# Kernel tuning notes

Measured on AMD Instinct MI355X. Metric: run time of the kernel, lower is better.

Reference implementation:

```python
import jax, jax.numpy as jnp
import numpy as np

EPS = 1e-6

def _layernorm(x, gamma, beta):
    # normalize over last dim (head_dim)
    mean = x.mean(axis=-1, keepdims=True)
    var = x.var(axis=-1, keepdims=True)
    return gamma * (x - mean) * jax.lax.rsqrt(var + EPS) + beta

def setup_inputs() -> dict:
    key = jax.random.key(0)
    ks = jax.random.split(key, 6)
    B, N, C, H = 2, 2048, 1024, 16
    Dh = C // H
    x = jax.random.normal(ks[0], (B, N, C), dtype=jnp.float32)
    qkv_w = jax.random.normal(ks[1], (C, 3 * C), dtype=jnp.float32) * (1.0 / np.sqrt(C))
    q_gamma = jnp.ones((Dh,), jnp.float32)
    q_beta = jnp.zeros((Dh,), jnp.float32)
    k_gamma = jnp.ones((Dh,), jnp.float32)
    k_beta = jnp.zeros((Dh,), jnp.float32)
    proj_w = jax.random.normal(ks[2], (C, C), dtype=jnp.float32) * (1.0 / np.sqrt(C))
    proj_b = jnp.zeros((C,), jnp.float32)
    return {"x": x, "qkv_w": qkv_w, "q_gamma": q_gamma, "q_beta": q_beta,
            "k_gamma": k_gamma, "k_beta": k_beta, "proj_w": proj_w, "proj_b": proj_b}

def reference(x, qkv_w, q_gamma, q_beta, k_gamma, k_beta, proj_w, proj_b):
    B, N, C = x.shape
    H = 16
    Dh = C // H
    scale = Dh ** -0.5
    qkv = x @ qkv_w                                   # [B,N,3C]
    qkv = qkv.reshape(B, N, 3, H, Dh)
    q = qkv[:, :, 0].transpose(0, 2, 1, 3)            # [B,H,N,Dh]
    k = qkv[:, :, 1].transpose(0, 2, 1, 3)
    v = qkv[:, :, 2].transpose(0, 2, 1, 3)
    q = _layernorm(q, q_gamma, q_beta)
    k = _layernorm(k, k_gamma, k_beta)
    attn = jnp.einsum('bhnd,bhmd->bhnm', q, k) * scale
    attn = jax.nn.softmax(attn, axis=-1)
    out = jnp.einsum('bhnm,bhmd->bhnd', attn, v)      # [B,H,N,Dh]
    out = out.transpose(0, 2, 1, 3).reshape(B, N, C)
    return out @ proj_w + proj_b
```

## Files before the change

### kernel.cpp

```cpp
#include <hip/hip_runtime.h>

typedef unsigned short u16;
typedef unsigned int u32;
typedef float f32x4 __attribute__((ext_vector_type(4)));
typedef float f32x16 __attribute__((ext_vector_type(16)));
typedef short s16x8 __attribute__((ext_vector_type(8)));

#define B_ 2
#define N_ 2048
#define C_ 1024
#define H_ 16
#define BN_ (B_*N_)

#define EXP2F(x) __builtin_amdgcn_exp2f(x)

__device__ __forceinline__ u16 f2bf(float f) {
  union { float f; unsigned u; } c; c.f = f;
  unsigned u = c.u;
  u = (u + 0x7fffu + ((u >> 16) & 1u)) >> 16;
  return (u16)u;
}
__device__ __forceinline__ float bf2f(u16 h) {
  union { unsigned u; float f; } c; c.u = ((unsigned)h) << 16;
  return c.f;
}
__device__ __forceinline__ u32 pack2(float lo, float hi) {
  u32 r;
  asm("v_cvt_pk_bf16_f32 %0, %1, %2" : "=v"(r) : "v"(lo), "v"(hi));
  return r;
}
__device__ __forceinline__ void gload16(const u16* g, u16* l) {
  __builtin_amdgcn_global_load_lds(
      (const __attribute__((address_space(1))) unsigned*)g,
      (__attribute__((address_space(3))) unsigned*)l, 16, 0, 0);
}

__global__ __launch_bounds__(256) void k_cast_bf16(const float* __restrict__ x,
                                                   u16* __restrict__ o, int n4) {
  int i = blockIdx.x * blockDim.x + threadIdx.x;
  if (i >= n4) return;
  float4 v = ((const float4*)x)[i];
  ushort4 r;
  r.x = f2bf(v.x); r.y = f2bf(v.y); r.z = f2bf(v.z); r.w = f2bf(v.w);
  ((ushort4*)o)[i] = r;
}

__global__ __launch_bounds__(256) void k_transpose_cast(const float* __restrict__ W,
                                                        u16* __restrict__ Wt,
                                                        int R, int Cc) {
  __shared__ float t[32][33];
  int tx = threadIdx.x, ty = threadIdx.y;
  int c0 = blockIdx.x * 32, r0 = blockIdx.y * 32;
#pragma unroll
  for (int i = 0; i < 4; ++i)
    t[ty + i * 8][tx] = W[(long)(r0 + ty + i * 8) * Cc + c0 + tx];
  __syncthreads();
#pragma unroll
  for (int i = 0; i < 4; ++i)
    Wt[(long)(c0 + ty + i * 8) * R + r0 + tx] = f2bf(t[tx][ty + i * 8]);
}

__global__ __launch_bounds__(256) void k_gemm_qkv_ln(const u16* __restrict__ A,
                                                     const u16* __restrict__ Bt,
                                                     const float* __restrict__ qg,
                                                     const float* __restrict__ qbeta,
                                                     const float* __restrict__ kg,
                                                     const float* __restrict__ kbeta,
                                                     u16* __restrict__ Qh,
                                                     u16* __restrict__ Kh,
                                                     u16* __restrict__ Vh) {
  const int K = C_;
  __shared__ u16 a_t[2][128 * 64];
  __shared__ u16 b_t[2][128 * 64];
  int tid = threadIdx.x;
  int w = tid >> 6, l = tid & 63;
  int l15 = l & 15, lhi = l >> 4;
  int wm = w >> 1, wn = w & 1;
  int rowA = l >> 3;
  int colA = ((l & 7) ^ (rowA & 7)) * 8;
  int x0 = (lhi ^ (l15 & 7)) * 8;
  int x1 = ((4 + lhi) ^ (l15 & 7)) * 8;
  const u16* Ab = A + (long)blockIdx.y * 128 * K;
  const u16* Bb = Bt + (long)blockIdx.x * 128 * K;
  f32x4 acc[4][4];
#pragma unroll
  for (int m = 0; m < 4; ++m)
#pragma unroll
    for (int n = 0; n < 4; ++n)
      acc[m][n] = (f32x4){0.f, 0.f, 0.f, 0.f};

  auto STAGE = [&](int k0, int bi) {
#pragma unroll
    for (int i = 0; i < 4; ++i) {
      int ci = i * 4 + w;
      gload16(Ab + (long)(ci * 8 + rowA) * K + k0 + colA, &a_t[bi][ci * 512]);
      gload16(Bb + (long)(ci * 8 + rowA) * K + k0 + colA, &b_t[bi][ci * 512]);
    }
  };

  const int NS = K / 64;
  STAGE(0, 0);
  for (int t = 0; t < NS; ++t) {
    __builtin_amdgcn_s_barrier();
    if (t + 1 < NS) {
      STAGE((t + 1) * 64, (t + 1) & 1);
      asm volatile("s_waitcnt vmcnt(8)" ::: "memory");
    } else {
      asm volatile("s_waitcnt vmcnt(0)" ::: "memory");
    }
    __builtin_amdgcn_s_barrier();
    const u16* at = a_t[t & 1];
    const u16* bt = b_t[t & 1];
#pragma unroll
    for (int kk = 0; kk < 2; ++kk) {
      int xo = kk ? x1 : x0;
      s16x8 af[4], bfr[4];
#pragma unroll
      for (int m = 0; m < 4; ++m)
        af[m] = *(const s16x8*)&at[(wm * 64 + m * 16 + l15) * 64 + xo];
#pragma unroll
      for (int n = 0; n < 4; ++n)
        bfr[n] = *(const s16x8*)&bt[(wn * 64 + n * 16 + l15) * 64 + xo];
#pragma unroll
      for (int m = 0; m < 4; ++m)
#pragma unroll
        for (int n = 0; n < 4; ++n)
          acc[m][n] = __builtin_amdgcn_mfma_f32_16x16x32_bf16(af[m], bfr[n], acc[m][n], 0, 0, 0);
    }
  }

  int cb = blockIdx.x * 128 + wn * 64;
  int s = cb >> 10;
  int h = (cb & 1023) >> 6;
  int rowbase = blockIdx.y * 128 + wm * 64;

  if (s == 2) {
#pragma unroll
    for (int m = 0; m < 4; ++m) {
#pragma unroll
      for (int r = 0; r < 4; ++r) {
        int row = rowbase + m * 16 + lhi * 4 + r;
        int b = row >> 11, nn = row & (N_ - 1);
        long ob = ((long)(b * H_ + h) * N_ + nn) * 64;
#pragma unroll
        for (int n = 0; n < 4; ++n)
          Vh[ob + n * 16 + l15] = f2bf(acc[m][n][r]);
      }
    }
  } else {
    const float* g = (s == 0) ? qg : kg;
    const float* be = (s == 0) ? qbeta : kbeta;
    u16* Oh = (s == 0) ? Qh : Kh;
    float sc = (s == 0) ? 0.125f * 1.44269504089f : 1.f;
    float gv[4], bv[4];
#pragma unroll
    for (int n = 0; n < 4; ++n) { gv[n] = g[n * 16 + l15]; bv[n] = be[n * 16 + l15]; }
#pragma unroll
    for (int m = 0; m < 4; ++m) {
#pragma unroll
      for (int r = 0; r < 4; ++r) {
        float t = (acc[m][0][r] + acc[m][1][r]) + (acc[m][2][r] + acc[m][3][r]);
        t += __shfl_xor(t, 1); t += __shfl_xor(t, 2);
        t += __shfl_xor(t, 4); t += __shfl_xor(t, 8);
        float mean = t * (1.f / 64.f);
        float v0 = acc[m][0][r] - mean, v1 = acc[m][1][r] - mean;
        float v2 = acc[m][2][r] - mean, v3 = acc[m][3][r] - mean;
        float q2 = (v0 * v0 + v1 * v1) + (v2 * v2 + v3 * v3);
        q2 += __shfl_xor(q2, 1); q2 += __shfl_xor(q2, 2);
        q2 += __shfl_xor(q2, 4); q2 += __shfl_xor(q2, 8);
        float rs = rsqrtf(q2 * (1.f / 64.f) + 1e-6f);
        int row = rowbase + m * 16 + lhi * 4 + r;
        int b = row >> 11, nn = row & (N_ - 1);
        long ob = ((long)(b * H_ + h) * N_ + nn) * 64;
        float vv[4] = {v0, v1, v2, v3};
#pragma unroll
        for (int n = 0; n < 4; ++n)
          Oh[ob + n * 16 + l15] = f2bf(sc * (gv[n] * vv[n] * rs + bv[n]));
      }
    }
  }
}

__global__ __launch_bounds__(256) void k_gemm_proj(const u16* __restrict__ A,
                                                   const u16* __restrict__ Bt,
                                                   float* __restrict__ Cout,
                                                   const float* __restrict__ bias,
                                                   int M, int N, int K) {
  __shared__ u16 a_t[2][128 * 64];
  __shared__ u16 b_t[2][128 * 64];
  int tid = threadIdx.x;
  int w = tid >> 6, l = tid & 63;
  int l15 = l & 15, lhi = l >> 4;
  int wm = w >> 1, wn = w & 1;
  int rowA = l >> 3;
  int colA = ((l & 7) ^ (rowA & 7)) * 8;
  int x0 = (lhi ^ (l15 & 7)) * 8;
  int x1 = ((4 + lhi) ^ (l15 & 7)) * 8;
  const u16* Ab = A + (long)blockIdx.y * 128 * K;
  const u16* Bb = Bt + (long)blockIdx.x * 128 * K;
  f32x4 acc[4][4];
#pragma unroll
  for (int m = 0; m < 4; ++m)
#pragma unroll
    for (int n = 0; n < 4; ++n)
      acc[m][n] = (f32x4){0.f, 0.f, 0.f, 0.f};

  auto STAGE = [&](int k0, int bi) {
#pragma unroll
    for (int i = 0; i < 4; ++i) {
      int ci = i * 4 + w;
      gload16(Ab + (long)(ci * 8 + rowA) * K + k0 + colA, &a_t[bi][ci * 512]);
      gload16(Bb + (long)(ci * 8 + rowA) * K + k0 + colA, &b_t[bi][ci * 512]);
    }
  };

  const int NS = 1024 / 64;
  STAGE(0, 0);
  for (int t = 0; t < NS; ++t) {
    __builtin_amdgcn_s_barrier();
    if (t + 1 < NS) {
      STAGE((t + 1) * 64, (t + 1) & 1);
      asm volatile("s_waitcnt vmcnt(8)" ::: "memory");
    } else {
      asm volatile("s_waitcnt vmcnt(0)" ::: "memory");
    }
    __builtin_amdgcn_s_barrier();
    const u16* at = a_t[t & 1];
    const u16* bt = b_t[t & 1];
#pragma unroll
    for (int kk = 0; kk < 2; ++kk) {
      int xo = kk ? x1 : x0;
      s16x8 af[4], bfr[4];
#pragma unroll
      for (int m = 0; m < 4; ++m)
        af[m] = *(const s16x8*)&at[(wm * 64 + m * 16 + l15) * 64 + xo];
#pragma unroll
      for (int n = 0; n < 4; ++n)
        bfr[n] = *(const s16x8*)&bt[(wn * 64 + n * 16 + l15) * 64 + xo];
#pragma unroll
      for (int m = 0; m < 4; ++m)
#pragma unroll
        for (int n = 0; n < 4; ++n)
          acc[m][n] = __builtin_amdgcn_mfma_f32_16x16x32_bf16(af[m], bfr[n], acc[m][n], 0, 0, 0);
    }
  }
#pragma unroll
  for (int m = 0; m < 4; ++m) {
#pragma unroll
    for (int n = 0; n < 4; ++n) {
      int col = blockIdx.x * 128 + wn * 64 + n * 16 + l15;
#pragma unroll
      for (int r = 0; r < 4; ++r) {
        int row = blockIdx.y * 128 + wm * 64 + m * 16 + lhi * 4 + r;
        Cout[(long)row * N + col] = acc[m][n][r] + bias[col];
      }
    }
  }
}

__global__ __launch_bounds__(512) void k_transpose_v(const u16* __restrict__ Vh,
                                                     u16* __restrict__ Vt) {
  __shared__ u16 t[64][65];
  int tx = threadIdx.x, ty = threadIdx.y;
  int bh = blockIdx.y;
  int n0 = blockIdx.x * 64;
#pragma unroll
  for (int i = 0; i < 8; ++i)
    t[ty + i * 8][tx] = Vh[((long)bh * N_ + n0 + ty + i * 8) * 64 + tx];
  __syncthreads();
#pragma unroll
  for (int i = 0; i < 8; ++i)
    Vt[((long)bh * 64 + ty + i * 8) * N_ + n0 + tx] = t[tx][ty + i * 8];
}

__global__ __launch_bounds__(512, 4) void k_attn(const u16* __restrict__ Qh,
                                                 const u16* __restrict__ Kh,
                                                 const u16* __restrict__ Vt,
                                                 u16* __restrict__ O) {
  __shared__ u16 k_t[2][2][64 * 64];
  __shared__ u16 v_t[2][2][64 * 64];
  int tid = threadIdx.x;
  int w = tid >> 6, l = tid & 63;
  int half = w >> 2, wq = w & 3;
  int l31 = l & 31, hi = l >> 5;
  int id = blockIdx.x;
  int swz = (id & 7) * 64 + (id >> 3);
  int bh = swz >> 4, qb = swz & 15;
  int b = bh >> 4, h = bh & 15;
  const u16* Qb = Qh + ((long)bh * N_ + qb * 128 + wq * 32) * 64;
  const u16* Kb = Kh + ((long)bh * N_ + half * 1024) * 64;
  const u16* Vb = Vt + (long)bh * 64 * N_ + half * 1024;

  s16x8 qf[4];
#pragma unroll
  for (int j = 0; j < 4; ++j)
    qf[j] = *(const s16x8*)&Qb[l31 * 64 + j * 16 + hi * 8];

  f32x16 acc0, acc1;
#pragma unroll
  for (int i = 0; i < 16; ++i) { acc0[i] = 0.f; acc1[i] = 0.f; }
  float lsum = 0.f;

  int off[2][4];
#pragma unroll
  for (int t = 0; t < 2; ++t)
#pragma unroll
    for (int j = 0; j < 4; ++j)
      off[t][j] = (t * 32 + l31) * 64 + (((j * 2 + hi) ^ (l & 7)) * 8);

  int srow = l >> 3;
  int scol = ((l & 7) ^ srow) * 8;

  auto STAGE = [&](int kt, int bi) {
#pragma unroll
    for (int i = 0; i < 2; ++i) {
      int ci = i * 4 + wq;
      gload16(Kb + (long)(kt + ci * 8 + srow) * 64 + scol, &k_t[half][bi][ci * 512]);
      gload16(Vb + (long)(ci * 8 + srow) * N_ + kt + scol, &v_t[half][bi][ci * 512]);
    }
  };

  const int NT = 16;
  STAGE(0, 0);

  for (int t = 0; t < NT; ++t) {
    __builtin_amdgcn_s_barrier();
    if (t + 1 < NT) {
      STAGE((t + 1) * 64, (t + 1) & 1);
      asm volatile("s_waitcnt vmcnt(4)" ::: "memory");
    } else {
      asm volatile("s_waitcnt vmcnt(0)" ::: "memory");
    }
    __builtin_amdgcn_s_barrier();
    const u16* kb = k_t[half][t & 1];
    const u16* vb = v_t[half][t & 1];

    f32x16 s0, s1;
#pragma unroll
    for (int i = 0; i < 16; ++i) { s0[i] = 0.f; s1[i] = 0.f; }
    __builtin_amdgcn_s_setprio(1);
#pragma unroll
    for (int j = 0; j < 4; ++j) {
      s16x8 kf0 = *(const s16x8*)&kb[off[0][j]];
      s0 = __builtin_amdgcn_mfma_f32_32x32x16_bf16(kf0, qf[j], s0, 0, 0, 0);
      s16x8 kf1 = *(const s16x8*)&kb[off[1][j]];
      s1 = __builtin_amdgcn_mfma_f32_32x32x16_bf16(kf1, qf[j], s1, 0, 0, 0);
    }
    __builtin_amdgcn_s_setprio(0);

#pragma unroll
    for (int i = 0; i < 16; ++i) {
      s0[i] = EXP2F(s0[i]);
      s1[i] = EXP2F(s1[i]);
    }
    f32x16 sm;
#pragma unroll
    for (int i = 0; i < 16; ++i) sm[i] = s0[i] + s1[i];
#pragma unroll
    for (int i = 0; i < 8; ++i) sm[i] += sm[i + 8];
#pragma unroll
    for (int i = 0; i < 4; ++i) sm[i] += sm[i + 4];
    float rs = (sm[0] + sm[1]) + (sm[2] + sm[3]);
    lsum += rs + __shfl_xor(rs, 32);

    s16x8 pa[4];
#pragma unroll
    for (int g = 0; g < 4; ++g) {
      const f32x16& sv = (g < 2) ? s0 : s1;
      int o = (g & 1) * 8;
      u32 w01 = pack2(sv[o + 0], sv[o + 1]);
      u32 w23 = pack2(sv[o + 2], sv[o + 3]);
      u32 w45 = pack2(sv[o + 4], sv[o + 5]);
      u32 w67 = pack2(sv[o + 6], sv[o + 7]);
      u32 recvA = __shfl_xor(hi ? w01 : w45, 32);
      u32 recvB = __shfl_xor(hi ? w23 : w67, 32);
      union { u32 u[4]; s16x8 v; } fr;
      fr.u[0] = hi ? recvA : w01;
      fr.u[1] = hi ? recvB : w23;
      fr.u[2] = hi ? w45 : recvA;
      fr.u[3] = hi ? w67 : recvB;
      pa[g] = fr.v;
    }

    __builtin_amdgcn_s_setprio(1);
#pragma unroll
    for (int j = 0; j < 4; ++j) {
      s16x8 vf0 = *(const s16x8*)&vb[off[0][j]];
      acc0 = __builtin_amdgcn_mfma_f32_32x32x16_bf16(pa[j], vf0, acc0, 0, 0, 0);
      s16x8 vf1 = *(const s16x8*)&vb[off[1][j]];
      acc1 = __builtin_amdgcn_mfma_f32_32x32x16_bf16(pa[j], vf1, acc1, 0, 0, 0);
    }
    __builtin_amdgcn_s_setprio(0);
  }

  __syncthreads();
  float* mbuf = (float*)&k_t[0][0][0];
  float* ml   = (float*)&v_t[0][0][0];

  if (half == 1) {
    if (hi == 0) ml[wq * 32 + l31] = lsum;
#pragma unroll
    for (int r = 0; r < 16; ++r) {
      mbuf[((wq * 32 + r) * 64) + l] = acc0[r];
      mbuf[((wq * 32 + 16 + r) * 64) + l] = acc1[r];
    }
  }
  __syncthreads();

  if (half == 0) {
    float s_b = ml[wq * 32 + l31];
    float lstar = lsum + s_b;
    int lsi = __float_as_int(lstar);
#pragma unroll
    for (int r = 0; r < 16; ++r) {
      int ql = (r & 3) + 8 * (r >> 2) + 4 * hi;
      float ls = __int_as_float(__builtin_amdgcn_ds_bpermute(ql << 2, lsi));
      float o0 = acc0[r] + mbuf[((wq * 32 + r) * 64) + l];
      float o1 = acc1[r] + mbuf[((wq * 32 + 16 + r) * 64) + l];
      float inv = 1.f / ls;
      int q = qb * 128 + wq * 32 + ql;
      long ob = ((long)(b * N_ + q) * H_ + h) * 64 + l31;
      O[ob] = f2bf(o0 * inv);
      O[ob + 32] = f2bf(o1 * inv);
    }
  }
}

extern "C" void kernel_launch(void* const* d_in, const int* in_sizes, int n_in,
                              void* d_out, int out_size, void* d_ws, size_t ws_size,
                              hipStream_t stream) {
  const float* x      = (const float*)d_in[0];
  const float* qkv_w  = (const float*)d_in[1];
  const float* q_g    = (const float*)d_in[2];
  const float* q_b    = (const float*)d_in[3];
  const float* k_g    = (const float*)d_in[4];
  const float* k_b    = (const float*)d_in[5];
  const float* proj_w = (const float*)d_in[6];
  const float* proj_b = (const float*)d_in[7];
  float* out = (float*)d_out;

  char* ws = (char*)d_ws;
  u16* xb     = (u16*)(ws + 0);
  u16* wqkvT  = (u16*)(ws + 8388608);
  u16* wprojT = (u16*)(ws + 14680064);
  u16* Qh     = (u16*)(ws + 16777216);
  u16* Kh     = (u16*)(ws + 25165824);
  u16* Vh     = (u16*)(ws + 33554432);
  u16* Vt     = (u16*)(ws + 41943040);
  u16* attnO  = xb;

  k_cast_bf16<<<4096, 256, 0, stream>>>(x, xb, (BN_ * C_) / 4);
  k_transpose_cast<<<dim3(96, 32), dim3(32, 8), 0, stream>>>(qkv_w, wqkvT, C_, 3 * C_);
  k_transpose_cast<<<dim3(32, 32), dim3(32, 8), 0, stream>>>(proj_w, wprojT, C_, C_);
  k_gemm_qkv_ln<<<dim3(24, 32), 256, 0, stream>>>(xb, wqkvT, q_g, q_b, k_g, k_b, Qh, Kh, Vh);
  k_transpose_v<<<dim3(32, 32), dim3(64, 8), 0, stream>>>(Vh, Vt);
  k_attn<<<512, 512, 0, stream>>>(Qh, Kh, Vt, attnO);
  k_gemm_proj<<<dim3(8, 32), 256, 0, stream>>>(attnO, wprojT, out, proj_b, BN_, C_, C_);
}
```

Baseline: 133.8 us.

## Fuse V transpose into QKV GEMM epilogue via shared-memory staging

The QKV GEMM epilogue for the V slice now stages the accumulator tile in shared memory, reusing the GEMM's LDS buffer, and writes V directly in transposed [bh, d, n] layout with 16-byte stores. This removes the separate transpose kernel launch and the round trip of V through global memory. The cost is an extra block barrier and some LDS traffic in the epilogue of the V blocks. pack2 is assumed to exist in the hidden helper code.

New measurement: 129.6 us. 1.03x faster.

```diff
diff --git a/kernel.cpp b/kernel.cpp
--- a/kernel.cpp
+++ b/kernel.cpp
@@ -68,10 +68,9 @@
                                                      const float* __restrict__ kbeta,
                                                      u16* __restrict__ Qh,
                                                      u16* __restrict__ Kh,
-                                                     u16* __restrict__ Vh) {
+                                                     u16* __restrict__ Vt) {
   const int K = C_;
-  __shared__ u16 a_t[2][128 * 64];
-  __shared__ u16 b_t[2][128 * 64];
+  __shared__ u16 smem[32768];
   int tid = threadIdx.x;
   int w = tid >> 6, l = tid & 63;
   int l15 = l & 15, lhi = l >> 4;
@@ -90,11 +89,13 @@
       acc[m][n] = (f32x4){0.f, 0.f, 0.f, 0.f};
 
   auto STAGE = [&](int k0, int bi) {
+    u16* at = smem + bi * 8192;
+    u16* bt = smem + 16384 + bi * 8192;
 #pragma unroll
     for (int i = 0; i < 4; ++i) {
       int ci = i * 4 + w;
-      gload16(Ab + (long)(ci * 8 + rowA) * K + k0 + colA, &a_t[bi][ci * 512]);
-      gload16(Bb + (long)(ci * 8 + rowA) * K + k0 + colA, &b_t[bi][ci * 512]);
+      gload16(Ab + (long)(ci * 8 + rowA) * K + k0 + colA, &at[ci * 512]);
+      gload16(Bb + (long)(ci * 8 + rowA) * K + k0 + colA, &bt[ci * 512]);
     }
   };
 
@@ -109,8 +110,8 @@
       asm volatile("s_waitcnt vmcnt(0)" ::: "memory");
     }
     __builtin_amdgcn_s_barrier();
-    const u16* at = a_t[t & 1];
-    const u16* bt = b_t[t & 1];
+    const u16* at = smem + (t & 1) * 8192;
+    const u16* bt = smem + 16384 + (t & 1) * 8192;
 #pragma unroll
     for (int kk = 0; kk < 2; ++kk) {
       int xo = kk ? x1 : x0;
@@ -135,17 +136,28 @@
   int rowbase = blockIdx.y * 128 + wm * 64;
 
   if (s == 2) {
-#pragma unroll
-    for (int m = 0; m < 4; ++m) {
-#pragma unroll
-      for (int r = 0; r < 4; ++r) {
-        int row = rowbase + m * 16 + lhi * 4 + r;
-        int b = row >> 11, nn = row & (N_ - 1);
-        long ob = ((long)(b * H_ + h) * N_ + nn) * 64;
-#pragma unroll
-        for (int n = 0; n < 4; ++n)
-          Vh[ob + n * 16 + l15] = f2bf(acc[m][n][r]);
+    __syncthreads();
+    u16* tbuf = smem + w * 4608;
+    u32* tb32 = (u32*)tbuf;
+#pragma unroll
+    for (int m = 0; m < 4; ++m)
+#pragma unroll
+      for (int n = 0; n < 4; ++n) {
+        int d = n * 16 + l15;
+#pragma unroll
+        for (int r = 0; r < 4; r += 2)
+          tb32[d * 36 + m * 8 + lhi * 2 + (r >> 1)] =
+              pack2(acc[m][n][r], acc[m][n][r + 1]);
       }
+    int b = rowbase >> 11;
+    int nnb = rowbase & (N_ - 1);
+    int bhv = b * H_ + h;
+    int ch = (l & 7) * 8;
+#pragma unroll
+    for (int i = 0; i < 8; ++i) {
+      int dl = i * 8 + (l >> 3);
+      s16x8 vv = *(const s16x8*)&tbuf[dl * 72 + ch];
+      *(s16x8*)&Vt[(long)(bhv * 64 + dl) * N_ + nnb + ch] = vv;
     }
   } else {
     const float* g = (s == 0) ? qg : kg;
@@ -258,21 +270,6 @@
   }
 }
 
-__global__ __launch_bounds__(512) void k_transpose_v(const u16* __restrict__ Vh,
-                                                     u16* __restrict__ Vt) {
-  __shared__ u16 t[64][65];
-  int tx = threadIdx.x, ty = threadIdx.y;
-  int bh = blockIdx.y;
-  int n0 = blockIdx.x * 64;
-#pragma unroll
-  for (int i = 0; i < 8; ++i)
-    t[ty + i * 8][tx] = Vh[((long)bh * N_ + n0 + ty + i * 8) * 64 + tx];
-  __syncthreads();
-#pragma unroll
-  for (int i = 0; i < 8; ++i)
-    Vt[((long)bh * 64 + ty + i * 8) * N_ + n0 + tx] = t[tx][ty + i * 8];
-}
-
 __global__ __launch_bounds__(512, 4) void k_attn(const u16* __restrict__ Qh,
                                                  const u16* __restrict__ Kh,
                                                  const u16* __restrict__ Vt,
@@ -445,15 +442,13 @@
   u16* wprojT = (u16*)(ws + 14680064);
   u16* Qh     = (u16*)(ws + 16777216);
   u16* Kh     = (u16*)(ws + 25165824);
-  u16* Vh     = (u16*)(ws + 33554432);
   u16* Vt     = (u16*)(ws + 41943040);
   u16* attnO  = xb;
 
   k_cast_bf16<<<4096, 256, 0, stream>>>(x, xb, (BN_ * C_) / 4);
   k_transpose_cast<<<dim3(96, 32), dim3(32, 8), 0, stream>>>(qkv_w, wqkvT, C_, 3 * C_);
   k_transpose_cast<<<dim3(32, 32), dim3(32, 8), 0, stream>>>(proj_w, wprojT, C_, C_);
-  k_gemm_qkv_ln<<<dim3(24, 32), 256, 0, stream>>>(xb, wqkvT, q_g, q_b, k_g, k_b, Qh, Kh, Vh);
-  k_transpose_v<<<dim3(32, 32), dim3(64, 8), 0, stream>>>(Vh, Vt);
+  k_gemm_qkv_ln<<<dim3(24, 32), 256, 0, stream>>>(xb, wqkvT, q_g, q_b, k_g, k_b, Qh, Kh, Vt);
   k_attn<<<512, 512, 0, stream>>>(Qh, Kh, Vt, attnO);
   k_gemm_proj<<<dim3(8, 32), 256, 0, stream>>>(attnO, wprojT, out, proj_b, BN_, C_, C_);
 }
```
